# Kernel optimization log

Measured on AMD Instinct MI355X. Metric: run time of the kernel, lower is better.

Reference implementation:

```python
import jax, jax.numpy as jnp
import numpy as np
import math

DIM = 1024
H = 16
HD = DIM // H  # 64
M = 64         # num_features
B, S = 4, 4096


def setup_inputs() -> dict:
    key = jax.random.key(0)
    ks = jax.random.split(key, 10)
    sc = 1.0 / math.sqrt(DIM)
    return {
        "x": jax.random.normal(ks[0], (B, S, DIM), dtype=jnp.float32),
        "Wq": jax.random.normal(ks[1], (DIM, DIM), dtype=jnp.float32) * sc,
        "bq": jax.random.normal(ks[2], (DIM,), dtype=jnp.float32) * 0.01,
        "Wk": jax.random.normal(ks[3], (DIM, DIM), dtype=jnp.float32) * sc,
        "bk": jax.random.normal(ks[4], (DIM,), dtype=jnp.float32) * 0.01,
        "Wv": jax.random.normal(ks[5], (DIM, DIM), dtype=jnp.float32) * sc,
        "bv": jax.random.normal(ks[6], (DIM,), dtype=jnp.float32) * 0.01,
        "Wo": jax.random.normal(ks[7], (DIM, DIM), dtype=jnp.float32) * sc,
        "bo": jax.random.normal(ks[8], (DIM,), dtype=jnp.float32) * 0.01,
        "P": jax.random.normal(ks[9], (H, M, HD), dtype=jnp.float32),
    }


def _feature_map(t, P):
    # t: [b,h,s,d], P: [h,m,d] -> relu(t @ P^T) / sqrt(m)
    proj = jnp.einsum("bhsd,hmd->bhsm", t, P)
    return jax.nn.relu(proj) * (1.0 / math.sqrt(P.shape[1]))


def reference(x, Wq, bq, Wk, bk, Wv, bv, Wo, bo, P):
    b, s, dim = x.shape
    h, m, hd = P.shape
    # Linear projections (torch Linear: x @ W^T + b), split heads -> [b,h,s,hd]
    def split_heads(y):
        return y.reshape(b, s, h, hd).transpose(0, 2, 1, 3)
    q = split_heads(x @ Wq.T + bq)
    k = split_heads(x @ Wk.T + bk)
    v = split_heads(x @ Wv.T + bv)
    q_prime = _feature_map(q, P)  # [b,h,s,m]
    k_prime = _feature_map(k, P)  # [b,h,s,m]
    kv = jnp.einsum("bhsm,bhsd->bhmd", k_prime, v)       # [b,h,m,hd]
    attn = jnp.einsum("bhsm,bhmd->bhsd", q_prime, kv)    # [b,h,s,hd]
    attn = attn.transpose(0, 2, 1, 3).reshape(b, s, dim)
    return attn @ Wo.T + bo
```

## Files before the change

kernel.cpp:

```cpp
#include <hip/hip_runtime.h>
#include <hip/hip_bf16.h>
#include <cstdint>

typedef __bf16 bf16_t;
typedef bf16_t bf16x8 __attribute__((ext_vector_type(8)));
typedef float f32x4 __attribute__((ext_vector_type(4)));


__device__ __forceinline__ void gload_lds16(const bf16_t* g, bf16_t* l) {
  __builtin_amdgcn_global_load_lds(
      (const __attribute__((address_space(1))) uint32_t*)g,
      (__attribute__((address_space(3))) uint32_t*)l, 16, 0, 0);
}

__global__ void cast_f32_bf16(const float* __restrict__ in, bf16_t* __restrict__ out, int n8) {
  int i = blockIdx.x * 256 + threadIdx.x;
  if (i < n8) {
    const f32x4* p = (const f32x4*)(in + (long)i * 8);
    f32x4 a = p[0], b = p[1];
    bf16x8 o;
#pragma unroll
    for (int j = 0; j < 4; ++j) { o[j] = (bf16_t)a[j]; o[j + 4] = (bf16_t)b[j]; }
    *(bf16x8*)(out + (long)i * 8) = o;
  }
}

__global__ void copy_f32(const float* __restrict__ in, float* __restrict__ out, int n) {
  int i = blockIdx.x * 256 + threadIdx.x;
  if (i < n) out[i] = in[i];
}

__global__ __launch_bounds__(256) void prep_wqk(
    const float* __restrict__ Wq, const float* __restrict__ bq,
    const float* __restrict__ Wk, const float* __restrict__ bk,
    const float* __restrict__ P,
    bf16_t* __restrict__ Wcat, float* __restrict__ bcat)
{
  int bid = blockIdx.x;
  int qk = bid >> 7, h = (bid >> 3) & 15, kt = bid & 7;
  const float* W = qk ? Wk : Wq;
  const float* bias = qk ? bk : bq;
  __shared__ float Pl[64 * 64];
  __shared__ float Wlt[128 * 68];
  int t = threadIdx.x;
  int k0 = kt * 128;
  for (int i = t * 4; i < 4096; i += 1024)
    *(f32x4*)&Pl[i] = *(const f32x4*)&P[h * 4096 + i];
  for (int fi = t; fi < 2048; fi += 256) {
    int row = fi >> 5;
    int c4 = fi & 31;
    f32x4 w = *(const f32x4*)&W[(long)(h * 64 + row) * 1024 + k0 + c4 * 4];
#pragma unroll
    for (int j = 0; j < 4; ++j) Wlt[(c4 * 4 + j) * 68 + row] = w[j];
  }
  __syncthreads();
  int kloc = t >> 1;
  int mh = (t & 1) * 32;
  for (int m = mh; m < mh + 32; ++m) {
    f32x4 s = {0.f, 0.f, 0.f, 0.f};
#pragma unroll
    for (int dd = 0; dd < 16; ++dd)
      s += (*(const f32x4*)&Pl[m * 64 + dd * 4]) * (*(const f32x4*)&Wlt[kloc * 68 + dd * 4]);
    float a = s[0] + s[1] + s[2] + s[3];
    Wcat[(long)(qk * 1024 + h * 64 + m) * 1024 + k0 + kloc] = (bf16_t)a;
  }
  if (kt == 0 && t < 64) {
    float a = 0.f;
    for (int d = 0; d < 64; ++d) a += Pl[t * 64 + d] * bias[h * 64 + d];
    bcat[qk * 1024 + h * 64 + t] = a;
  }
}

#define WAITV(N) asm volatile("s_waitcnt vmcnt(" #N ")" ::: "memory")
#define BAR() __builtin_amdgcn_s_barrier()

#define STAGE(sAn, sBn, KOFF) {                                   \
  gload_lds16(A  + a_off[0] + (KOFF), &sAn[dst8]);                \
  gload_lds16(A  + a_off[1] + (KOFF), &sAn[4096 + dst8]);         \
  gload_lds16(A  + a_off[2] + (KOFF), &sAn[8192 + dst8]);         \
  gload_lds16(A  + a_off[3] + (KOFF), &sAn[12288 + dst8]);        \
  gload_lds16(Bm + b_off[0] + (KOFF), &sBn[dst8]);                \
  gload_lds16(Bm + b_off[1] + (KOFF), &sBn[4096 + dst8]);         \
  gload_lds16(Bm + b_off[2] + (KOFF), &sBn[8192 + dst8]);         \
  gload_lds16(Bm + b_off[3] + (KOFF), &sBn[12288 + dst8]);        \
}

#define COMPUTE(sAc, sBc) {                                                             \
  bf16x8 bfr[4][2], afr[4][2];                                                          \
  _Pragma("unroll") for (int ni = 0; ni < 4; ++ni) {                                    \
    bfr[ni][0] = *(const bf16x8*)&sBc[bbase + ni * 1024 + aoff0];                       \
    bfr[ni][1] = *(const bf16x8*)&sBc[bbase + ni * 1024 + aoff1];                       \
  }                                                                                     \
  _Pragma("unroll") for (int mi = 0; mi < 4; ++mi) {                                    \
    afr[mi][0] = *(const bf16x8*)&sAc[abase + mi * 1024 + aoff0];                       \
    afr[mi][1] = *(const bf16x8*)&sAc[abase + mi * 1024 + aoff1];                       \
  }                                                                                     \
  __builtin_amdgcn_s_setprio(1);                                                        \
  _Pragma("unroll") for (int mi = 0; mi < 4; ++mi)                                      \
    _Pragma("unroll") for (int ni = 0; ni < 4; ++ni) {                                  \
      acc[mi][ni] = __builtin_amdgcn_mfma_f32_16x16x32_bf16(afr[mi][0], bfr[ni][0], acc[mi][ni], 0, 0, 0); \
      acc[mi][ni] = __builtin_amdgcn_mfma_f32_16x16x32_bf16(afr[mi][1], bfr[ni][1], acc[mi][ni], 0, 0, 0); \
    }                                                                                   \
  __builtin_amdgcn_s_setprio(0);                                                        \
  _Pragma("unroll") for (int mi = 0; mi < 4; ++mi) {                                    \
    afr[mi][0] = *(const bf16x8*)&sAc[abase + (mi + 4) * 1024 + aoff0];                 \
    afr[mi][1] = *(const bf16x8*)&sAc[abase + (mi + 4) * 1024 + aoff1];                 \
  }                                                                                     \
  __builtin_amdgcn_s_setprio(1);                                                        \
  _Pragma("unroll") for (int mi = 0; mi < 4; ++mi)                                      \
    _Pragma("unroll") for (int ni = 0; ni < 4; ++ni) {                                  \
      acc[mi + 4][ni] = __builtin_amdgcn_mfma_f32_16x16x32_bf16(afr[mi][0], bfr[ni][0], acc[mi + 4][ni], 0, 0, 0); \
      acc[mi + 4][ni] = __builtin_amdgcn_mfma_f32_16x16x32_bf16(afr[mi][1], bfr[ni][1], acc[mi + 4][ni], 0, 0, 0); \
    }                                                                                   \
  __builtin_amdgcn_s_setprio(0);                                                        \
}

template <int EPI>
__global__ __launch_bounds__(512, 2) void gemm256(
    const bf16_t* __restrict__ A, int lda,
    const bf16_t* __restrict__ B0, int ldb,
    const float* __restrict__ bias,
    void* __restrict__ Cv, int ldc,
    int K, int ncols, int cpx,
    int rows_per_batch, long bstride)
{
  __shared__ alignas(16) bf16_t sA0[16384], sA1[16384];
  __shared__ alignas(16) bf16_t sB0[16384], sB1[16384];

  const int lin = blockIdx.x;
  const int wgid = (lin & 7) * cpx + (lin >> 3);
  const int row0 = (wgid / ncols) * 256;
  const int col0 = (wgid % ncols) * 256;

  const int tid = threadIdx.x;
  const int w = tid >> 6, l = tid & 63;
  const int wr = w >> 2, wc = w & 3;
  const int llo = l & 15, lhi = l >> 4;
  const int x7 = llo & 7;

  const bf16_t* Bm = B0 + (long)(row0 / rows_per_batch) * bstride;

  long a_off[4], b_off[4];
#pragma unroll
  for (int i = 0; i < 4; ++i) {
    int c = i * 512 + tid;
    int r = c >> 3;
    int kqs = (c & 7) ^ (r & 7);
    a_off[i] = (long)(row0 + r) * lda + kqs * 8;
    b_off[i] = (long)(col0 + r) * ldb + kqs * 8;
  }
  const int dst8 = tid * 8;

  const int aoff0 = ((lhi)     ^ x7) * 8;
  const int aoff1 = ((lhi + 4) ^ x7) * 8;
  const int abase = (wr * 128 + llo) * 64;
  const int bbase = (wc * 64 + llo) * 64;

  f32x4 acc[8][4] = {};
  const int NT = K >> 6;

  STAGE(sA0, sB0, 0L);
  STAGE(sA1, sB1, 64L);

  int t = 0;
  for (; t + 2 < NT; t += 2) {
    WAITV(8); BAR();
    COMPUTE(sA0, sB0);
    BAR();
    STAGE(sA0, sB0, (long)(t + 2) * 64);
    WAITV(8); BAR();
    COMPUTE(sA1, sB1);
    BAR();
    STAGE(sA1, sB1, (long)(t + 3) * 64);
  }
  WAITV(8); BAR();
  COMPUTE(sA0, sB0);
  BAR();
  WAITV(0); BAR();
  COMPUTE(sA1, sB1);

#pragma unroll
  for (int ni = 0; ni < 4; ++ni) {
    const int gcol = col0 + wc * 64 + ni * 16 + llo;
    const float bz = bias[gcol];
#pragma unroll
    for (int mi = 0; mi < 8; ++mi) {
      const int grow0 = row0 + wr * 128 + mi * 16 + lhi * 4;
#pragma unroll
      for (int j = 0; j < 4; ++j) {
        float v = acc[mi][ni][j] + bz;
        if constexpr (EPI == 1) { if (gcol < 2048) v = fmaxf(v, 0.f) * 0.125f; }
        if constexpr (EPI == 2)
          ((float*)Cv)[(long)(grow0 + j) * ldc + gcol] = v;
        else
          ((bf16_t*)Cv)[(long)(grow0 + j) * ldc + gcol] = (bf16_t)v;
      }
    }
  }
}

__global__ __launch_bounds__(256) void kv_partial(
    const bf16_t* __restrict__ QKV, float* __restrict__ kvpart)
{
  int bh = blockIdx.x;
  int split = blockIdx.y;
  int b = bh >> 4, h = bh & 15;
  __shared__ alignas(16) bf16_t Kt[64 * 32];
  __shared__ alignas(16) bf16_t Vt[64 * 32];
  int t = threadIdx.x;
  int wv = t >> 6, lane = t & 63, lhi = lane >> 4, llo = lane & 15;
  int r = t >> 3;
  int c = (t & 7) * 8;
  f32x4 acc[4] = {};
  long rowbase = ((long)b * 4096 + split * 512) * 3072 + h * 64 + c;
  for (int sc = 0; sc < 16; ++sc) {
    long off = rowbase + (long)(sc * 32 + r) * 3072;
    bf16x8 kk = *(const bf16x8*)(QKV + off + 1024);
    bf16x8 vvv = *(const bf16x8*)(QKV + off + 2048);
#pragma unroll
    for (int j = 0; j < 8; ++j) {
      Kt[(c + j) * 32 + r] = kk[j];
      Vt[(c + j) * 32 + r] = vvv[j];
    }
    __syncthreads();
    bf16x8 a = *(const bf16x8*)&Kt[(wv * 16 + llo) * 32 + lhi * 8];
#pragma unroll
    for (int ni = 0; ni < 4; ++ni) {
      bf16x8 bb = *(const bf16x8*)&Vt[(ni * 16 + llo) * 32 + lhi * 8];
      acc[ni] = __builtin_amdgcn_mfma_f32_16x16x32_bf16(a, bb, acc[ni], 0, 0, 0);
    }
    __syncthreads();
  }
#pragma unroll
  for (int ni = 0; ni < 4; ++ni)
#pragma unroll
    for (int j = 0; j < 4; ++j) {
      int m = wv * 16 + lhi * 4 + j;
      int d = ni * 16 + llo;
      kvpart[((long)split * 64 + bh) * 4096 + m * 64 + d] = acc[ni][j];
    }
}

__global__ void kv_reduce(const float* __restrict__ part, float* __restrict__ kv) {
  int i = blockIdx.x * 256 + threadIdx.x;
  float s = 0.f;
#pragma unroll
  for (int sp = 0; sp < 8; ++sp) s += part[sp * 262144 + i];
  kv[i] = s;
}

__global__ __launch_bounds__(256) void wcombt_kernel(
    const float* __restrict__ kv, const float* __restrict__ Wo,
    bf16_t* __restrict__ WcT)
{
  int nt = blockIdx.x, h = blockIdx.y, b = blockIdx.z;
  __shared__ float kvs[4096];
  int t = threadIdx.x;
  for (int i = t * 4; i < 4096; i += 1024)
    *(f32x4*)&kvs[i] = *(const f32x4*)&kv[((long)b * 16 + h) * 4096 + i];
  __syncthreads();
  int n = nt * 128 + (t >> 1);
  int mh = (t & 1) * 32;
  f32x4 wo[16];
#pragma unroll
  for (int dd = 0; dd < 16; ++dd) wo[dd] = *(const f32x4*)&Wo[(long)n * 1024 + h * 64 + dd * 4];
  for (int m = mh; m < mh + 32; ++m) {
    f32x4 s = {0.f, 0.f, 0.f, 0.f};
#pragma unroll
    for (int dd = 0; dd < 16; ++dd)
      s += (*(const f32x4*)&kvs[m * 64 + dd * 4]) * wo[dd];
    WcT[((long)b * 1024 + n) * 1024 + h * 64 + m] = (bf16_t)(s[0] + s[1] + s[2] + s[3]);
  }
}

extern "C" void kernel_launch(void* const* d_in, const int* in_sizes, int n_in,
                              void* d_out, int out_size, void* d_ws, size_t ws_size,
                              hipStream_t stream) {
  (void)in_sizes; (void)n_in; (void)out_size; (void)ws_size;
  const float* x  = (const float*)d_in[0];
  const float* Wq = (const float*)d_in[1];
  const float* bq = (const float*)d_in[2];
  const float* Wk = (const float*)d_in[3];
  const float* bk = (const float*)d_in[4];
  const float* Wv = (const float*)d_in[5];
  const float* bv = (const float*)d_in[6];
  const float* Wo = (const float*)d_in[7];
  const float* bo = (const float*)d_in[8];
  const float* P  = (const float*)d_in[9];
  float* out = (float*)d_out;

  char* ws = (char*)d_ws;
  bf16_t* xb     = (bf16_t*)(ws + 0);
  bf16_t* QKV    = (bf16_t*)(ws + 33554432);
  bf16_t* Wcat   = (bf16_t*)(ws + 134217728);
  float*  bcat   = (float*) (ws + 140509184);
  float*  kvpart = (float*) (ws + 140521472);
  float*  kvbuf  = (float*) (ws + 148910080);
  bf16_t* WcT    = (bf16_t*)(ws + 149958656);

  cast_f32_bf16<<<8192, 256, 0, stream>>>(x, xb, 2097152);
  cast_f32_bf16<<<512, 256, 0, stream>>>(Wv, Wcat + (size_t)2048 * 1024, 131072);
  copy_f32<<<4, 256, 0, stream>>>(bv, bcat + 2048, 1024);
  prep_wqk<<<256, 256, 0, stream>>>(Wq, bq, Wk, bk, P, Wcat, bcat);

  gemm256<1><<<768, 512, 0, stream>>>(
      xb, 1024, Wcat, 1024, bcat, QKV, 3072, 1024, 12, 96, 1 << 30, 0);

  kv_partial<<<dim3(64, 8), 256, 0, stream>>>(QKV, kvpart);
  kv_reduce<<<1024, 256, 0, stream>>>(kvpart, kvbuf);

  wcombt_kernel<<<dim3(8, 16, 4), 256, 0, stream>>>(kvbuf, Wo, WcT);

  gemm256<2><<<256, 512, 0, stream>>>(
      QKV, 3072, WcT, 1024, bo, out, 1024, 1024, 4, 32, 4096, (long)1024 * 1024);
}
```

Baseline: 246.2 us.

## Load GEMM B operand directly to registers and stage bf16 epilogue through LDS

The 256x256 GEMM now stages only A through LDS and has each wave load its B fragments straight from global memory into double-buffered registers, prefetching the next k-tile while the current one computes. LDS is merged into one buffer, and the bf16 epilogue writes results into swizzled shared memory, then stores coalesced 16-byte rows. The intent is to cut LDS traffic and LDS-load latency for B and to replace scattered 2-byte global stores. In exchange, B is read redundantly by every wave row, which raises global/L2 traffic and register pressure. Synchronisation switches from explicit vmcnt waits to __syncthreads.

```diff
diff --git a/kernel.cpp b/kernel.cpp
--- a/kernel.cpp
+++ b/kernel.cpp
@@ -71,35 +71,31 @@
   }
 }
 
-#define WAITV(N) asm volatile("s_waitcnt vmcnt(" #N ")" ::: "memory")
-#define BAR() __builtin_amdgcn_s_barrier()
-
-#define STAGE(sAn, sBn, KOFF) {                                   \
-  gload_lds16(A  + a_off[0] + (KOFF), &sAn[dst8]);                \
-  gload_lds16(A  + a_off[1] + (KOFF), &sAn[4096 + dst8]);         \
-  gload_lds16(A  + a_off[2] + (KOFF), &sAn[8192 + dst8]);         \
-  gload_lds16(A  + a_off[3] + (KOFF), &sAn[12288 + dst8]);        \
-  gload_lds16(Bm + b_off[0] + (KOFF), &sBn[dst8]);                \
-  gload_lds16(Bm + b_off[1] + (KOFF), &sBn[4096 + dst8]);         \
-  gload_lds16(Bm + b_off[2] + (KOFF), &sBn[8192 + dst8]);         \
-  gload_lds16(Bm + b_off[3] + (KOFF), &sBn[12288 + dst8]);        \
-}
-
-#define COMPUTE(sAc, sBc) {                                                             \
-  bf16x8 bfr[4][2], afr[4][2];                                                          \
-  _Pragma("unroll") for (int ni = 0; ni < 4; ++ni) {                                    \
-    bfr[ni][0] = *(const bf16x8*)&sBc[bbase + ni * 1024 + aoff0];                       \
-    bfr[ni][1] = *(const bf16x8*)&sBc[bbase + ni * 1024 + aoff1];                       \
-  }                                                                                     \
+
+#define LOADB(dst, KN) {                                                     \
+  _Pragma("unroll") for (int ni = 0; ni < 4; ++ni) {                         \
+    dst[ni][0] = *(const bf16x8*)(Bp + (long)ni * 16 * ldb + (KN));          \
+    dst[ni][1] = *(const bf16x8*)(Bp + (long)ni * 16 * ldb + (KN) + 32);     \
+  } }
+
+#define TILE1(sAc, sAn, bC, bN, KN, STG) {                                              \
+  bf16x8 afr[4][2];                                                                     \
   _Pragma("unroll") for (int mi = 0; mi < 4; ++mi) {                                    \
     afr[mi][0] = *(const bf16x8*)&sAc[abase + mi * 1024 + aoff0];                       \
     afr[mi][1] = *(const bf16x8*)&sAc[abase + mi * 1024 + aoff1];                       \
   }                                                                                     \
+  if (STG) {                                                                            \
+    gload_lds16(A + a_off[0] + (KN), &sAn[dst8]);                                       \
+    gload_lds16(A + a_off[1] + (KN), &sAn[4096 + dst8]);                                \
+    gload_lds16(A + a_off[2] + (KN), &sAn[8192 + dst8]);                                \
+    gload_lds16(A + a_off[3] + (KN), &sAn[12288 + dst8]);                               \
+    LOADB(bN, KN);                                                                      \
+  }                                                                                     \
   __builtin_amdgcn_s_setprio(1);                                                        \
   _Pragma("unroll") for (int mi = 0; mi < 4; ++mi)                                      \
     _Pragma("unroll") for (int ni = 0; ni < 4; ++ni) {                                  \
-      acc[mi][ni] = __builtin_amdgcn_mfma_f32_16x16x32_bf16(afr[mi][0], bfr[ni][0], acc[mi][ni], 0, 0, 0); \
-      acc[mi][ni] = __builtin_amdgcn_mfma_f32_16x16x32_bf16(afr[mi][1], bfr[ni][1], acc[mi][ni], 0, 0, 0); \
+      acc[mi][ni] = __builtin_amdgcn_mfma_f32_16x16x32_bf16(afr[mi][0], bC[ni][0], acc[mi][ni], 0, 0, 0); \
+      acc[mi][ni] = __builtin_amdgcn_mfma_f32_16x16x32_bf16(afr[mi][1], bC[ni][1], acc[mi][ni], 0, 0, 0); \
     }                                                                                   \
   __builtin_amdgcn_s_setprio(0);                                                        \
   _Pragma("unroll") for (int mi = 0; mi < 4; ++mi) {                                    \
@@ -109,10 +105,11 @@
   __builtin_amdgcn_s_setprio(1);                                                        \
   _Pragma("unroll") for (int mi = 0; mi < 4; ++mi)                                      \
     _Pragma("unroll") for (int ni = 0; ni < 4; ++ni) {                                  \
-      acc[mi + 4][ni] = __builtin_amdgcn_mfma_f32_16x16x32_bf16(afr[mi][0], bfr[ni][0], acc[mi + 4][ni], 0, 0, 0); \
-      acc[mi + 4][ni] = __builtin_amdgcn_mfma_f32_16x16x32_bf16(afr[mi][1], bfr[ni][1], acc[mi + 4][ni], 0, 0, 0); \
+      acc[mi + 4][ni] = __builtin_amdgcn_mfma_f32_16x16x32_bf16(afr[mi][0], bC[ni][0], acc[mi + 4][ni], 0, 0, 0); \
+      acc[mi + 4][ni] = __builtin_amdgcn_mfma_f32_16x16x32_bf16(afr[mi][1], bC[ni][1], acc[mi + 4][ni], 0, 0, 0); \
     }                                                                                   \
   __builtin_amdgcn_s_setprio(0);                                                        \
+  __syncthreads();                                                                      \
 }
 
 template <int EPI>
@@ -124,8 +121,9 @@
     int K, int ncols, int cpx,
     int rows_per_batch, long bstride)
 {
-  __shared__ alignas(16) bf16_t sA0[16384], sA1[16384];
-  __shared__ alignas(16) bf16_t sB0[16384], sB1[16384];
+  __shared__ alignas(16) bf16_t smem[65536];
+  bf16_t* const sA0 = smem;
+  bf16_t* const sA1 = smem + 16384;
 
   const int lin = blockIdx.x;
   const int wgid = (lin & 7) * cpx + (lin >> 3);
@@ -139,61 +137,79 @@
   const int x7 = llo & 7;
 
   const bf16_t* Bm = B0 + (long)(row0 / rows_per_batch) * bstride;
-
-  long a_off[4], b_off[4];
+  const bf16_t* Bp = Bm + (long)(col0 + wc * 64 + llo) * ldb + lhi * 8;
+
+  long a_off[4];
 #pragma unroll
   for (int i = 0; i < 4; ++i) {
     int c = i * 512 + tid;
     int r = c >> 3;
     int kqs = (c & 7) ^ (r & 7);
     a_off[i] = (long)(row0 + r) * lda + kqs * 8;
-    b_off[i] = (long)(col0 + r) * ldb + kqs * 8;
   }
   const int dst8 = tid * 8;
 
   const int aoff0 = ((lhi)     ^ x7) * 8;
   const int aoff1 = ((lhi + 4) ^ x7) * 8;
   const int abase = (wr * 128 + llo) * 64;
-  const int bbase = (wc * 64 + llo) * 64;
 
   f32x4 acc[8][4] = {};
+  bf16x8 bfrA[4][2], bfrB[4][2];
   const int NT = K >> 6;
 
-  STAGE(sA0, sB0, 0L);
-  STAGE(sA1, sB1, 64L);
+  gload_lds16(A + a_off[0], &sA0[dst8]);
+  gload_lds16(A + a_off[1], &sA0[4096 + dst8]);
+  gload_lds16(A + a_off[2], &sA0[8192 + dst8]);
+  gload_lds16(A + a_off[3], &sA0[12288 + dst8]);
+  LOADB(bfrA, 0L);
+  __syncthreads();
 
   int t = 0;
   for (; t + 2 < NT; t += 2) {
-    WAITV(8); BAR();
-    COMPUTE(sA0, sB0);
-    BAR();
-    STAGE(sA0, sB0, (long)(t + 2) * 64);
-    WAITV(8); BAR();
-    COMPUTE(sA1, sB1);
-    BAR();
-    STAGE(sA1, sB1, (long)(t + 3) * 64);
-  }
-  WAITV(8); BAR();
-  COMPUTE(sA0, sB0);
-  BAR();
-  WAITV(0); BAR();
-  COMPUTE(sA1, sB1);
-
-#pragma unroll
-  for (int ni = 0; ni < 4; ++ni) {
-    const int gcol = col0 + wc * 64 + ni * 16 + llo;
-    const float bz = bias[gcol];
-#pragma unroll
-    for (int mi = 0; mi < 8; ++mi) {
-      const int grow0 = row0 + wr * 128 + mi * 16 + lhi * 4;
-#pragma unroll
-      for (int j = 0; j < 4; ++j) {
-        float v = acc[mi][ni][j] + bz;
-        if constexpr (EPI == 1) { if (gcol < 2048) v = fmaxf(v, 0.f) * 0.125f; }
-        if constexpr (EPI == 2)
-          ((float*)Cv)[(long)(grow0 + j) * ldc + gcol] = v;
-        else
-          ((bf16_t*)Cv)[(long)(grow0 + j) * ldc + gcol] = (bf16_t)v;
+    TILE1(sA0, sA1, bfrA, bfrB, (long)(t + 1) * 64, 1);
+    TILE1(sA1, sA0, bfrB, bfrA, (long)(t + 2) * 64, 1);
+  }
+  TILE1(sA0, sA1, bfrA, bfrB, (long)(NT - 1) * 64, 1);
+  TILE1(sA1, sA0, bfrB, bfrA, 0L, 0);
+
+  if constexpr (EPI == 1) {
+#pragma unroll
+    for (int ni = 0; ni < 4; ++ni) {
+      const int cc = wc * 64 + ni * 16 + llo;
+      const int gcol = col0 + cc;
+      const float bz = bias[gcol];
+      const bool doRelu = gcol < 2048;
+#pragma unroll
+      for (int mi = 0; mi < 8; ++mi) {
+#pragma unroll
+        for (int j = 0; j < 4; ++j) {
+          const int rr = wr * 128 + mi * 16 + lhi * 4 + j;
+          float v = acc[mi][ni][j] + bz;
+          if (doRelu) v = fmaxf(v, 0.f) * 0.125f;
+          smem[rr * 256 + (((cc >> 3) ^ (rr & 31)) << 3) + (cc & 7)] = (bf16_t)v;
+        }
+      }
+    }
+    __syncthreads();
+    const int r = tid >> 1, half = tid & 1;
+    bf16_t* outp = (bf16_t*)Cv + (long)(row0 + r) * ldc + col0;
+#pragma unroll
+    for (int k = 0; k < 16; ++k) {
+      const int c = half * 16 + k;
+      bf16x8 vv = *(const bf16x8*)&smem[r * 256 + ((c ^ (r & 31)) << 3)];
+      *(bf16x8*)(outp + c * 8) = vv;
+    }
+  } else {
+#pragma unroll
+    for (int ni = 0; ni < 4; ++ni) {
+      const int gcol = col0 + wc * 64 + ni * 16 + llo;
+      const float bz = bias[gcol];
+#pragma unroll
+      for (int mi = 0; mi < 8; ++mi) {
+        const int grow0 = row0 + wr * 128 + mi * 16 + lhi * 4;
+#pragma unroll
+        for (int j = 0; j < 4; ++j)
+          ((float*)Cv)[(long)(grow0 + j) * ldc + gcol] = acc[mi][ni][j] + bz;
       }
     }
   }
```

Measured after the change: 332.1 us. +34.9%, slower.
